# Kernel tuning notes

Hardware: AMD Instinct MI355X
Metric: run time of the kernel (lower is better)

The kernel has to match this reference:

```python
import jax, jax.numpy as jnp
import numpy as np

N_TRAIN = 2000
N_ATOMS = 21
DIM_D = N_ATOMS * (N_ATOMS - 1) // 2   # 210 pairwise descriptors
DIM_I = 3 * N_ATOMS                    # 63 Cartesian force dims
N_PERMS = 12
N_COLS = 8
SIG = 10.0

_TRIL_ROWS, _TRIL_COLS = np.tril_indices(N_ATOMS, k=-1)


def setup_inputs() -> dict:
    key = jax.random.key(0)
    k1, k2 = jax.random.split(key)
    R_desc = jax.random.normal(k1, (N_TRAIN, DIM_D), dtype=jnp.float32)
    R_d_desc = jax.random.normal(k2, (N_TRAIN, DIM_D, 3), dtype=jnp.float32)
    rng = np.random.default_rng(0)
    # permutation table: identity first, then random symmetry perms of descriptor rows
    perms = np.stack([np.arange(DIM_D)] + [rng.permutation(DIM_D) for _ in range(N_PERMS - 1)])  # (P, D)
    # linear indices into a tiled (P copies) descriptor, laid out so that
    # tril_perms_lin.reshape(DIM_D, N_PERMS)[k, p] = perms[p, k] + p*DIM_D (matches sGDML)
    tril_perms_lin = (perms.T + np.arange(N_PERMS)[None, :] * DIM_D).ravel()
    j_idxs = rng.integers(0, N_TRAIN, size=N_COLS)
    return {
        "R_desc": R_desc,
        "R_d_desc": R_d_desc,
        "tril_perms_lin": jnp.asarray(tril_perms_lin, dtype=jnp.int32),
        "j_idxs": jnp.asarray(j_idxs, dtype=jnp.int32),
    }


def _d_desc_full(d_comp):
    """Expand compact pairwise Jacobian (N, D, 3) to full (N, D, 3*A).
    Pair row k for atoms (a,b) gets +d in atom a's slot and -d in atom b's slot."""
    n = d_comp.shape[0]
    out = jnp.zeros((n, DIM_D, N_ATOMS, 3), d_comp.dtype)
    k = jnp.arange(DIM_D)
    out = out.at[:, k, _TRIL_ROWS].set(d_comp)
    out = out.at[:, k, _TRIL_COLS].set(-d_comp)
    return out.reshape(n, DIM_D, DIM_I)


def reference(R_desc, R_d_desc, tril_perms_lin, j_idxs):
    sqrt5 = np.sqrt(5.0).astype(np.float32)
    base_div = 3.0 * SIG ** 4
    # indexing a P-fold tiled array of length D is equivalent to mod D
    perm_idx = jnp.reshape(tril_perms_lin, (DIM_D, N_PERMS)).T % DIM_D  # (P, D)
    Rd_full = _d_desc_full(R_d_desc)  # (N, D, I)

    def column_block(j):
        rj_desc_perms = R_desc[j][perm_idx]        # (P, D)  permuted descriptor of point j
        rj_d_perms = Rd_full[j][perm_idx]          # (P, D, I) permuted Jacobian of point j
        diff = R_desc[:, None, :] - rj_desc_perms[None, :, :]   # (N, P, D)
        norm = sqrt5 * jnp.linalg.norm(diff, axis=-1)            # (N, P)
        mat52 = jnp.exp(-norm / SIG) * (5.0 / base_div)          # (N, P)
        b = jnp.einsum('npd,pde->npe', diff, rj_d_perms)         # (N, P, I)
        outer = jnp.einsum('npd,npe->nde', diff * (5.0 * mat52)[..., None], b)  # (N, D, I)
        outer = outer - jnp.einsum('pde,np->nde', rj_d_perms, (SIG ** 2 + SIG * norm) * mat52)
        kblk = jnp.einsum('nde,ndk->nke', outer, Rd_full)        # (N, I_row, I_col)
        return kblk.reshape(N_TRAIN * DIM_I, DIM_I)

    K = jax.vmap(column_block)(j_idxs)                 # (nJ, N*I, I)
    K = jnp.transpose(K, (1, 0, 2)).reshape(N_TRAIN * DIM_I, N_COLS * DIM_I)
    return K
```

## Files before the change

### kernel.cpp

```cpp
#include <hip/hip_runtime.h>
#include <hip/hip_fp16.h>
#include <math.h>

#define NTRAIN 2000
#define DIMD 210
#define DIMI 63
#define NPERM 12
#define NCOLS 8
#define NATOM 21
#define SIGF 10.0f

#define WS_PERM      0
#define WS_PAIRROW   5040
#define WS_PAIRCOL   5250
#define WS_GTAB      6300
#define WS_ENTOFF    11340
#define WS_ENTS      11782
#define WS_TILEMAP   21862
#define WS_PERMAB    22304
#define A_INT_OFF    25088
#define A_BYTE_OFF   (A_INT_OFF * 4)
#define A_PER_N      (64 * 224)
#define A_BYTES      ((size_t)NTRAIN * A_PER_N * 2)
#define WS_NEEDED    ((size_t)A_BYTE_OFF + A_BYTES)

typedef _Float16 f16x8 __attribute__((ext_vector_type(8)));
typedef float f32x4 __attribute__((ext_vector_type(4)));

__global__ __launch_bounds__(512) void gdml_setup(const int* __restrict__ tril,
                                                  int* __restrict__ ws, int wsBig) {
  __shared__ int sPerm[NPERM * DIMD];
  __shared__ int sInv[NPERM * DIMD];
  __shared__ int sRow[DIMD], sCol[DIMD];
  __shared__ int sPairs[NATOM * 20], sNeg[NATOM * 20];
  __shared__ int sCnt[441];
  __shared__ int sScan[512];
  __shared__ int sOff[442];

  const int tid = threadIdx.x;

  for (int d = tid; d < DIMD; d += 512) {
    int a = 1;
    while ((a * (a + 1)) / 2 <= d) a++;
    sRow[d] = a;
    sCol[d] = d - (a * (a - 1)) / 2;
  }
  for (int idx = tid; idx < NPERM * DIMD; idx += 512) {
    int p = idx / DIMD, d = idx % DIMD;
    sPerm[idx] = tril[d * NPERM + p] % DIMD;
  }
  __syncthreads();
  for (int idx = tid; idx < NPERM * DIMD; idx += 512) {
    int p = idx / DIMD;
    sInv[p * DIMD + sPerm[idx]] = idx % DIMD;
  }
  if (tid < NATOM) {
    int t = tid, c = 0;
    for (int d = 0; d < DIMD; ++d) {
      if (sRow[d] == t)      { sPairs[t * 20 + c] = d; sNeg[t * 20 + c] = 0; c++; }
      else if (sCol[d] == t) { sPairs[t * 20 + c] = d; sNeg[t * 20 + c] = 1; c++; }
    }
  }
  __syncthreads();

  for (int idx = tid; idx < NPERM * NATOM * 20; idx += 512) {
    int p = idx / (NATOM * 20);
    int r = idx % (NATOM * 20);
    int d = sPairs[r], neg = sNeg[r];
    int tw = sInv[p * DIMD + d];
    int pd = sPerm[p * DIMD + d];
    ws[WS_GTAB + idx] = d | (tw << 9) | (pd << 18) | (neg << 27);
  }

  if (wsBig) {
    for (int idx = tid; idx < NPERM * DIMD; idx += 512) {
      int dd = sPerm[idx];
      ws[WS_PERMAB + idx] = dd | (sRow[dd] << 8) | (sCol[dd] << 13);
    }
    return;
  }

  for (int idx = tid; idx < NPERM * DIMD; idx += 512) ws[WS_PERM + idx] = sPerm[idx];

  for (int q = tid; q < 441; q += 512) {
    int A = q / NATOM, B = q % NATOM, c = 0;
    for (int i = 0; i < 20; ++i) {
      int d = sPairs[A * 20 + i];
      for (int p = 0; p < NPERM; ++p) {
        int dd = sPerm[p * DIMD + d];
        c += (sRow[dd] == B) + (sCol[dd] == B);
      }
    }
    sCnt[q] = c;
  }
  __syncthreads();

  sScan[tid] = (tid < 441) ? sCnt[tid] : 0;
  __syncthreads();
  for (int s = 1; s < 512; s <<= 1) {
    int v = (tid >= s) ? sScan[tid - s] : 0;
    __syncthreads();
    sScan[tid] += v;
    __syncthreads();
  }
  if (tid == 0) sOff[0] = 0;
  if (tid < 441) sOff[tid + 1] = sScan[tid];
  __syncthreads();
  for (int q = tid; q < 442; q += 512) ws[WS_ENTOFF + q] = sOff[q];

  for (int q = tid; q < 441; q += 512) {
    int c = sCnt[q], r = 0;
    for (int q2 = 0; q2 < 441; ++q2) {
      int c2v = sCnt[q2];
      r += (c2v > c) || (c2v == c && q2 < q);
    }
    ws[WS_TILEMAP + r] = q;
  }

  for (int q = tid; q < 441; q += 512) {
    int A = q / NATOM, B = q % NATOM;
    int o = sOff[q];
    for (int i = 0; i < 20; ++i) {
      int d = sPairs[A * 20 + i];
      int negA = sNeg[A * 20 + i];
      for (int p = 0; p < NPERM; ++p) {
        int dd = sPerm[p * DIMD + d];
        int base = (d << 3) | (dd << 15) | (p << 26);
        if (sRow[dd] == B) ws[WS_ENTS + (o++)] = base | ((negA ^ 1) << 30);
        if (sCol[dd] == B) ws[WS_ENTS + (o++)] = base | (negA << 30);
      }
    }
  }
}

__global__ __launch_bounds__(256) void build_A(const float* __restrict__ R_d_desc,
                                               int* __restrict__ ws) {
  const int bid = blockIdx.x;
  const int n = (bid & 7) * (NTRAIN / 8) + (bid >> 3);
  const int* gtab = ws + WS_GTAB;
  _Float16* A = (_Float16*)((char*)ws + A_BYTE_OFF) + (size_t)n * A_PER_N;
  const float* rd = R_d_desc + (size_t)n * (DIMD * 3);
  const int tid = threadIdx.x;

  f16x8 z = {0, 0, 0, 0, 0, 0, 0, 0};
  for (int u = tid; u < 64 * 28; u += 256) ((f16x8*)A)[u] = z;
  __syncthreads();

  for (int u = tid; u < NATOM * 20; u += 256) {
    int v = gtab[u];
    int d = v & 511;
    float s = (v & (1 << 27)) ? -1.0f : 1.0f;
    int at = u / 20;
    A[(3 * at + 0) * 224 + d] = (_Float16)(s * rd[3 * d + 0]);
    A[(3 * at + 1) * 224 + d] = (_Float16)(s * rd[3 * d + 1]);
    A[(3 * at + 2) * 224 + d] = (_Float16)(s * rd[3 * d + 2]);
  }
}

__device__ inline unsigned h16(float f) {
  return (unsigned)__half_as_ushort(__float2half_rn(f));
}
__device__ inline float uh(unsigned u) {
  return __half2float(__ushort_as_half((unsigned short)(u & 0xFFFFu)));
}
__device__ inline int tswz(int r, int e) {
  return r * 64 + ((((e >> 3) ^ r) & 7) << 3) + (e & 7);
}
__device__ inline float pick3(uint2 v, int u) {
  return (u == 0) ? uh(v.x) : (u == 1) ? uh(v.x >> 16) : uh(v.y);
}

#define MT_STRIDE 232

__global__ __launch_bounds__(256, 4) void gdml_main_mfma(
    const float* __restrict__ R_desc, const float* __restrict__ R_d_desc,
    const int* __restrict__ j_idxs, const int* __restrict__ ws,
    float* __restrict__ out) {
  const int* gtab   = ws + WS_GTAB;
  const int* permAB = ws + WS_PERMAB;

  const int bid = blockIdx.x;
  const int x = bid & 7;
  const int t = bid >> 3;
  const int n = x * (NTRAIN / 8) + (t >> 3);
  const int jc = t & 7;
  const int tid = threadIdx.x;
  const int j = j_idxs[jc];

  __shared__ __align__(16) _Float16 MT[64 * MT_STRIDE];
  __shared__ uint2 Rdn2[DIMD];
  __shared__ uint2 Rdj2[DIMD];
  __shared__ __align__(16) _Float16 Gk[64][16];
  __shared__ float c1s[NPERM], c2s[NPERM];
  __shared__ float2 RnRj[DIMD];
  __shared__ float partial[252];

  if (tid < DIMD) {
    RnRj[tid] = make_float2(R_desc[(size_t)n * DIMD + tid],
                            R_desc[(size_t)j * DIMD + tid]);
    const float* gn = R_d_desc + (size_t)n * (DIMD * 3) + 3 * tid;
    const float* gj = R_d_desc + (size_t)j * (DIMD * 3) + 3 * tid;
    Rdn2[tid] = make_uint2(h16(gn[0]) | (h16(gn[1]) << 16), h16(gn[2]));
    Rdj2[tid] = make_uint2(h16(gj[0]) | (h16(gj[1]) << 16), h16(gj[2]));
  }
  {
    float4 zf = make_float4(0.f, 0.f, 0.f, 0.f);
    float4* mz = (float4*)MT;
    for (int i = tid; i < 64 * MT_STRIDE * 2 / 16; i += 256) mz[i] = zf;
    f16x8 z8 = {0, 0, 0, 0, 0, 0, 0, 0};
    for (int i = tid; i < 128; i += 256) ((f16x8*)Gk)[i] = z8;
  }
  __syncthreads();

  float g0 = 0, g1 = 0, g2 = 0, b0 = 0, b1 = 0, b2 = 0;
  int bp = 0, bat = 0;
  if (tid < NPERM * NATOM) {
    bp = tid / NATOM; bat = tid - bp * NATOM;
    const int* gt = &gtab[(bp * NATOM + bat) * 20];
    float nacc = 0.f;
#pragma unroll
    for (int i = 0; i < 20; ++i) {
      int v = gt[i];
      int d = v & 511, tw = (v >> 9) & 511, pd = (v >> 18) & 511;
      unsigned sg = ((unsigned)(v & (1 << 27))) << 4;
      float2 rrd = RnRj[d];
      float diff_d = rrd.x - RnRj[pd].y;
      float diff_tw = RnRj[tw].x - rrd.y;
      float fd = __uint_as_float(__float_as_uint(diff_d) ^ sg);
      float ftw = __uint_as_float(__float_as_uint(diff_tw) ^ sg);
      nacc += diff_d * diff_d;
      uint2 rn = Rdn2[d];
      uint2 rj = Rdj2[d];
      g0 += uh(rn.x) * fd;  g1 += uh(rn.x >> 16) * fd;  g2 += uh(rn.y) * fd;
      b0 += uh(rj.x) * ftw; b1 += uh(rj.x >> 16) * ftw; b2 += uh(rj.y) * ftw;
    }
    partial[tid] = nacc;
  }
  __syncthreads();

  if (tid < NPERM) {
    float s = 0.f;
#pragma unroll
    for (int i = 0; i < 21; ++i) s += partial[tid * 21 + i];
    s *= 0.5f;
    float nrm = sqrtf(5.0f) * sqrtf(s);
    float mat52 = expf(-nrm / SIGF) * (5.0f / (3.0f * SIGF * SIGF * SIGF * SIGF));
    c1s[tid] = 5.0f * mat52;
    c2s[tid] = (SIGF * SIGF + SIGF * nrm) * mat52;
  }
  __syncthreads();

  if (tid < NPERM * NATOM) {
    float c1 = c1s[bp];
    Gk[3 * bat + 0][4 + bp] = (_Float16)(c1 * g0);
    Gk[3 * bat + 1][4 + bp] = (_Float16)(c1 * g1);
    Gk[3 * bat + 2][4 + bp] = (_Float16)(c1 * g2);
    MT[(3 * bat + 0) * MT_STRIDE + 212 + bp] = (_Float16)b0;
    MT[(3 * bat + 1) * MT_STRIDE + 212 + bp] = (_Float16)b1;
    MT[(3 * bat + 2) * MT_STRIDE + 212 + bp] = (_Float16)b2;
  }
  if (tid < DIMD) {
    int d = tid;
    _Float16* m = MT + d;
#pragma unroll
    for (int p = 0; p < NPERM; ++p) {
      int v = permAB[p * DIMD + d];
      int dd = v & 255, a = (v >> 8) & 31, b = (v >> 13) & 31;
      float c2 = c2s[p];
      uint2 rj = Rdj2[dd];
      float v0 = c2 * uh(rj.x), v1 = c2 * uh(rj.x >> 16), v2 = c2 * uh(rj.y);
      int ca = (3 * a) * MT_STRIDE, cb = (3 * b) * MT_STRIDE;
      m[ca] = (_Float16)((float)m[ca] - v0);
      m[ca + MT_STRIDE] = (_Float16)((float)m[ca + MT_STRIDE] - v1);
      m[ca + 2 * MT_STRIDE] = (_Float16)((float)m[ca + 2 * MT_STRIDE] - v2);
      m[cb] = (_Float16)((float)m[cb] + v0);
      m[cb + MT_STRIDE] = (_Float16)((float)m[cb + MT_STRIDE] + v1);
      m[cb + 2 * MT_STRIDE] = (_Float16)((float)m[cb + 2 * MT_STRIDE] + v2);
    }
  } else {
    for (int r = tid - DIMD; r < DIMI; r += 256 - DIMD) {
      int at = r / 3, u = r - 3 * at;
      float v208 = (at == 20) ? pick3(Rdn2[208], u)
                 : (at == 18) ? -pick3(Rdn2[208], u) : 0.f;
      float v209 = (at == 20) ? pick3(Rdn2[209], u)
                 : (at == 19) ? -pick3(Rdn2[209], u) : 0.f;
      Gk[r][0] = (_Float16)v208;
      Gk[r][1] = (_Float16)v209;
    }
  }
  __syncthreads();

  f32x4 acc0 = {0.f, 0.f, 0.f, 0.f}, acc1 = acc0, acc2 = acc0, acc3 = acc0;
  const int lane = tid & 63;
  const int nt = tid >> 6;
  const int ci = lane & 15;
  const int kOct = lane >> 4;
  const _Float16* Ag = (const _Float16*)((const char*)ws + A_BYTE_OFF)
                       + (size_t)n * A_PER_N;
  const _Float16* aBase = Ag + ci * 224 + kOct * 8;
  const _Float16* mBase = &MT[(16 * nt + ci) * MT_STRIDE + kOct * 8];
  {
    f16x8 bf_c = *(const f16x8*)(mBase);
    f16x8 a0_c = *(const f16x8*)(aBase);
    f16x8 a1_c = *(const f16x8*)(aBase + 16 * 224);
    f16x8 a2_c = *(const f16x8*)(aBase + 32 * 224);
    f16x8 a3_c = *(const f16x8*)(aBase + 48 * 224);
#pragma unroll
    for (int kk = 0; kk < 6; ++kk) {
      f16x8 bf_n, a0_n, a1_n, a2_n, a3_n;
      if (kk < 5) {
        bf_n = *(const f16x8*)(mBase + (kk + 1) * 32);
        a0_n = *(const f16x8*)(aBase + (kk + 1) * 32);
        a1_n = *(const f16x8*)(aBase + 16 * 224 + (kk + 1) * 32);
        a2_n = *(const f16x8*)(aBase + 32 * 224 + (kk + 1) * 32);
        a3_n = *(const f16x8*)(aBase + 48 * 224 + (kk + 1) * 32);
      }
      acc0 = __builtin_amdgcn_mfma_f32_16x16x32_f16(a0_c, bf_c, acc0, 0, 0, 0);
      acc1 = __builtin_amdgcn_mfma_f32_16x16x32_f16(a1_c, bf_c, acc1, 0, 0, 0);
      acc2 = __builtin_amdgcn_mfma_f32_16x16x32_f16(a2_c, bf_c, acc2, 0, 0, 0);
      acc3 = __builtin_amdgcn_mfma_f32_16x16x32_f16(a3_c, bf_c, acc3, 0, 0, 0);
      if (kk < 5) {
        bf_c = bf_n; a0_c = a0_n; a1_c = a1_n; a2_c = a2_n; a3_c = a3_n;
      }
    }
    f16x8 bf6 = *(const f16x8*)(mBase + 6 * 32);
    f16x8 a0, a1, a2, a3;
    if (kOct >= 2) {
      int off = (kOct - 2) * 8;
      a0 = *(const f16x8*)&Gk[ci][off];
      a1 = *(const f16x8*)&Gk[16 + ci][off];
      a2 = *(const f16x8*)&Gk[32 + ci][off];
      a3 = *(const f16x8*)&Gk[48 + ci][off];
    } else {
      a0 = *(const f16x8*)(aBase + 6 * 32);
      a1 = *(const f16x8*)(aBase + 16 * 224 + 6 * 32);
      a2 = *(const f16x8*)(aBase + 32 * 224 + 6 * 32);
      a3 = *(const f16x8*)(aBase + 48 * 224 + 6 * 32);
    }
    acc0 = __builtin_amdgcn_mfma_f32_16x16x32_f16(a0, bf6, acc0, 0, 0, 0);
    acc1 = __builtin_amdgcn_mfma_f32_16x16x32_f16(a1, bf6, acc1, 0, 0, 0);
    acc2 = __builtin_amdgcn_mfma_f32_16x16x32_f16(a2, bf6, acc2, 0, 0, 0);
    acc3 = __builtin_amdgcn_mfma_f32_16x16x32_f16(a3, bf6, acc3, 0, 0, 0);
  }

  {
    const int c = 16 * nt + ci;
    if (c < DIMI) {
      const size_t base = (size_t)n * DIMI * (NCOLS * DIMI) + (size_t)jc * DIMI;
      float* ob = out + base + c;
      const int rb = kOct * 4;
#pragma unroll
      for (int r8 = 0; r8 < 4; ++r8) {
        int r = rb + r8;
        ob[(size_t)r * (NCOLS * DIMI)] = acc0[r8];
        ob[(size_t)(16 + r) * (NCOLS * DIMI)] = acc1[r8];
        ob[(size_t)(32 + r) * (NCOLS * DIMI)] = acc2[r8];
        if (48 + r < DIMI) ob[(size_t)(48 + r) * (NCOLS * DIMI)] = acc3[r8];
      }
    }
  }
}

__global__ __launch_bounds__(256, 8) void gdml_main_csr(
    const float* __restrict__ R_desc, const float* __restrict__ R_d_desc,
    const int* __restrict__ j_idxs, const int* __restrict__ ws,
    float* __restrict__ out) {
  const int* perm    = ws + WS_PERM;
  const int* gtab    = ws + WS_GTAB;
  const int* entOff  = ws + WS_ENTOFF;
  const int* ents    = ws + WS_ENTS;
  const int* tileMap = ws + WS_TILEMAP;

  const int bid = blockIdx.x;
  const int jc = bid & 7;
  const int n = bid >> 3;
  const int tid = threadIdx.x;
  const int j = j_idxs[jc];

  __shared__ uint2 Rdn2[DIMD];
  __shared__ uint2 Rdj2[DIMD];
  __shared__ __align__(16) float GT[NPERM][64];
  __shared__ __align__(16) float bT[NPERM][64];
  __shared__ float c1s[NPERM], c2s[NPERM];
  __shared__ __align__(16) char uni[DIMI * 64 * 2];
  float* Rn = (float*)uni;
  float* Rj = Rn + DIMD;
  float* partial = Rj + DIMD;
  ushort* tileH = (ushort*)uni;

  for (int i = tid; i < DIMD; i += 256) {
    Rn[i] = R_desc[(size_t)n * DIMD + i];
    Rj[i] = R_desc[(size_t)j * DIMD + i];
  }
  if (tid < DIMD) {
    const float* gn = R_d_desc + (size_t)n * (DIMD * 3) + 3 * tid;
    const float* gj = R_d_desc + (size_t)j * (DIMD * 3) + 3 * tid;
    Rdn2[tid] = make_uint2(h16(gn[0]) | (h16(gn[1]) << 16), h16(gn[2]));
    Rdj2[tid] = make_uint2(h16(gj[0]) | (h16(gj[1]) << 16), h16(gj[2]));
  }
  __syncthreads();

  if (tid < 252) {
    int p = tid / 21, seg = tid % 21;
    const int* pp = &perm[p * DIMD + seg * 10];
    const float* rn = &Rn[seg * 10];
    float s = 0.f;
#pragma unroll
    for (int i = 0; i < 10; ++i) {
      float v = rn[i] - Rj[pp[i]];
      s += v * v;
    }
    partial[tid] = s;
  }
  __syncthreads();
  if (tid < NPERM) {
    float s = 0.f;
#pragma unroll
    for (int i = 0; i < 21; ++i) s += partial[tid * 21 + i];
    float nrm = sqrtf(5.0f) * sqrtf(s);
    float mat52 = expf(-nrm / SIGF) * (5.0f / (3.0f * SIGF * SIGF * SIGF * SIGF));
    c1s[tid] = 5.0f * mat52;
    c2s[tid] = (SIGF * SIGF + SIGF * nrm) * mat52;
  }
  __syncthreads();

  if (tid < NPERM * NATOM) {
    int p = tid / NATOM, at = tid % NATOM;
    const int* gt = &gtab[(p * NATOM + at) * 20];
    float g0 = 0, g1 = 0, g2 = 0, b0 = 0, b1 = 0, b2 = 0;
#pragma unroll
    for (int i = 0; i < 20; ++i) {
      int v = gt[i];
      int d = v & 511, tw = (v >> 9) & 511, pd = (v >> 18) & 511;
      unsigned sg = ((unsigned)(v & (1 << 27))) << 4;
      float fd = __uint_as_float(__float_as_uint(Rn[d] - Rj[pd]) ^ sg);
      float ftw = __uint_as_float(__float_as_uint(Rn[tw] - Rj[d]) ^ sg);
      uint2 rn = Rdn2[d];
      uint2 rj = Rdj2[d];
      g0 += uh(rn.x) * fd;  g1 += uh(rn.x >> 16) * fd;  g2 += uh(rn.y) * fd;
      b0 += uh(rj.x) * ftw; b1 += uh(rj.x >> 16) * ftw; b2 += uh(rj.y) * ftw;
    }
    float c1 = c1s[p];
    GT[p][3 * at + 0] = c1 * g0;
    GT[p][3 * at + 1] = c1 * g1;
    GT[p][3 * at + 2] = c1 * g2;
    bT[p][3 * at + 0] = b0;
    bT[p][3 * at + 1] = b1;
    bT[p][3 * at + 2] = b2;
  }
  __syncthreads();

  for (int s = 0; s < 2; ++s) {
    int rank;
    if (s == 0) { if (tid > 220) break; rank = tid; }
    else        { if (tid >= 220) break; rank = 440 - tid; }
    int q = tileMap[rank];
    int A = q / NATOM, B = q % NATOM;
    float acc[3][3];
#pragma unroll
    for (int c = 0; c < 3; ++c)
#pragma unroll
      for (int e = 0; e < 3; ++e) acc[c][e] = 0.f;

    int o0 = entOff[q], o1 = entOff[q + 1];
    for (int o = o0; o < o1; ++o) {
      int v = ents[o];
      int d8  = v & 0xFF8;
      int dd8 = (v >> 12) & 0xFF8;
      int p4  = (v >> 24) & 0x3C;
      unsigned sgn = ((unsigned)v & 0x40000000u) << 1;
      float c2 = __uint_as_float(
          __float_as_uint(*(const float*)((const char*)c2s + p4)) ^ sgn);
      uint2 rn = *(const uint2*)((const char*)Rdn2 + d8);
      uint2 rj = *(const uint2*)((const char*)Rdj2 + dd8);
      float nx = uh(rn.x), ny = uh(rn.x >> 16), nz = uh(rn.y);
      float w0 = c2 * uh(rj.x), w1 = c2 * uh(rj.x >> 16), w2 = c2 * uh(rj.y);
      acc[0][0] += nx * w0; acc[0][1] += nx * w1; acc[0][2] += nx * w2;
      acc[1][0] += ny * w0; acc[1][1] += ny * w1; acc[1][2] += ny * w2;
      acc[2][0] += nz * w0; acc[2][1] += nz * w1; acc[2][2] += nz * w2;
    }
#pragma unroll
    for (int cg = 0; cg < 3; ++cg) {
      int r = 3 * A + cg;
#pragma unroll
      for (int u = 0; u < 3; ++u)
        tileH[tswz(r, 3 * B + u)] = (ushort)h16(acc[cg][u]);
    }
  }
  __syncthreads();

  const size_t base = (size_t)n * DIMI * (NCOLS * DIMI) + (size_t)jc * DIMI;
  if (tid < 252) {
    int k = tid >> 2, ec = tid & 3;
    int e0 = ec * 16;
    const uint4* q0 = (const uint4*)&tileH[k * 64 + (((2 * ec) ^ k) & 7) * 8];
    const uint4* q1 = (const uint4*)&tileH[k * 64 + (((2 * ec + 1) ^ k) & 7) * 8];
    uint4 u0 = *q0, u1 = *q1;
    float acc[16];
    acc[0] = uh(u0.x);  acc[1] = uh(u0.x >> 16);
    acc[2] = uh(u0.y);  acc[3] = uh(u0.y >> 16);
    acc[4] = uh(u0.z);  acc[5] = uh(u0.z >> 16);
    acc[6] = uh(u0.w);  acc[7] = uh(u0.w >> 16);
    acc[8] = uh(u1.x);  acc[9] = uh(u1.x >> 16);
    acc[10] = uh(u1.y); acc[11] = uh(u1.y >> 16);
    acc[12] = uh(u1.z); acc[13] = uh(u1.z >> 16);
    acc[14] = uh(u1.w); acc[15] = uh(u1.w >> 16);
#pragma unroll
    for (int p = 0; p < NPERM; ++p) {
      float g = GT[p][k];
      const float4* bp = (const float4*)&bT[p][e0];
      float4 b0 = bp[0], b1 = bp[1], b2 = bp[2], b3 = bp[3];
      acc[0] += g * b0.x;  acc[1] += g * b0.y;  acc[2] += g * b0.z;  acc[3] += g * b0.w;
      acc[4] += g * b1.x;  acc[5] += g * b1.y;  acc[6] += g * b1.z;  acc[7] += g * b1.w;
      acc[8] += g * b2.x;  acc[9] += g * b2.y;  acc[10] += g * b2.z; acc[11] += g * b2.w;
      acc[12] += g * b3.x; acc[13] += g * b3.y; acc[14] += g * b3.z; acc[15] += g * b3.w;
    }
    float* op = out + base + (size_t)k * (NCOLS * DIMI) + e0;
    const int lim = DIMI - e0;
#pragma unroll
    for (int i = 0; i < 16; ++i)
      if (i < lim) op[i] = acc[i];
  }
}

extern "C" void kernel_launch(void* const* d_in, const int* in_sizes, int n_in,
                              void* d_out, int out_size, void* d_ws, size_t ws_size,
                              hipStream_t stream) {
  const float* R_desc = (const float*)d_in[0];
  const float* R_d_desc = (const float*)d_in[1];
  const int* tril = (const int*)d_in[2];
  const int* j_idxs = (const int*)d_in[3];
  float* out = (float*)d_out;
  int* ws = (int*)d_ws;

  const int wsBig = (ws_size >= WS_NEEDED) ? 1 : 0;
  hipLaunchKernelGGL(gdml_setup, dim3(1), dim3(512), 0, stream, tril, ws, wsBig);
  if (wsBig) {
    hipLaunchKernelGGL(build_A, dim3(NTRAIN), dim3(256), 0, stream, R_d_desc, ws);
    hipLaunchKernelGGL(gdml_main_mfma, dim3(NTRAIN * NCOLS), dim3(256), 0, stream,
                       R_desc, R_d_desc, j_idxs, ws, out);
  } else {
    hipLaunchKernelGGL(gdml_main_csr, dim3(NTRAIN * NCOLS), dim3(256), 0, stream,
                       R_desc, R_d_desc, j_idxs, ws, out);
  }
}
```

Measured before the change: 282.1 us.

## Compute permuted G and B projections with MFMA instead of scalar gather loops

The per-permutation projections g (diff times the Jacobian of n) and b (permuted diff times the Jacobian of j) are now built as small matrix products on the MFMA units. The kernel first stores fp16 diff and permuted-diff tiles in shared memory, then multiplies them against the precomputed expanded Jacobian tables. Before, each thread ran a 20-step gather over a pair table in scalar code. The change reuses the MT buffer for the diff tiles, so it adds extra zeroing passes and barriers. It also drops the Rdn2 staging and the manual software prefetch in the main MFMA loop, and it adds fp16 rounding of the diffs before the projections.

```diff
diff --git a/kernel.cpp b/kernel.cpp
--- a/kernel.cpp
+++ b/kernel.cpp
@@ -11,8 +11,6 @@
 #define SIGF 10.0f
 
 #define WS_PERM      0
-#define WS_PAIRROW   5040
-#define WS_PAIRCOL   5250
 #define WS_GTAB      6300
 #define WS_ENTOFF    11340
 #define WS_ENTS      11782
@@ -74,6 +72,7 @@
 
   if (wsBig) {
     for (int idx = tid; idx < NPERM * DIMD; idx += 512) {
+      ws[WS_PERM + idx] = sPerm[idx] | (sInv[idx] << 9);
       int dd = sPerm[idx];
       ws[WS_PERMAB + idx] = dd | (sRow[dd] << 8) | (sCol[dd] << 13);
     }
@@ -166,17 +165,15 @@
 __device__ inline int tswz(int r, int e) {
   return r * 64 + ((((e >> 3) ^ r) & 7) << 3) + (e & 7);
 }
-__device__ inline float pick3(uint2 v, int u) {
-  return (u == 0) ? uh(v.x) : (u == 1) ? uh(v.x >> 16) : uh(v.y);
-}
 
 #define MT_STRIDE 232
+#define DIF_HALVES (16 * MT_STRIDE)
 
 __global__ __launch_bounds__(256, 4) void gdml_main_mfma(
     const float* __restrict__ R_desc, const float* __restrict__ R_d_desc,
     const int* __restrict__ j_idxs, const int* __restrict__ ws,
     float* __restrict__ out) {
-  const int* gtab   = ws + WS_GTAB;
+  const int* ptab   = ws + WS_PERM;
   const int* permAB = ws + WS_PERMAB;
 
   const int bid = blockIdx.x;
@@ -188,51 +185,48 @@
   const int j = j_idxs[jc];
 
   __shared__ __align__(16) _Float16 MT[64 * MT_STRIDE];
-  __shared__ uint2 Rdn2[DIMD];
+  _Float16* Dif  = MT;
+  _Float16* DifP = MT + DIF_HALVES;
   __shared__ uint2 Rdj2[DIMD];
   __shared__ __align__(16) _Float16 Gk[64][16];
   __shared__ float c1s[NPERM], c2s[NPERM];
   __shared__ float2 RnRj[DIMD];
   __shared__ float partial[252];
 
+  const _Float16* Atab = (const _Float16*)((const char*)ws + A_BYTE_OFF);
+
   if (tid < DIMD) {
     RnRj[tid] = make_float2(R_desc[(size_t)n * DIMD + tid],
                             R_desc[(size_t)j * DIMD + tid]);
-    const float* gn = R_d_desc + (size_t)n * (DIMD * 3) + 3 * tid;
     const float* gj = R_d_desc + (size_t)j * (DIMD * 3) + 3 * tid;
-    Rdn2[tid] = make_uint2(h16(gn[0]) | (h16(gn[1]) << 16), h16(gn[2]));
     Rdj2[tid] = make_uint2(h16(gj[0]) | (h16(gj[1]) << 16), h16(gj[2]));
   }
   {
-    float4 zf = make_float4(0.f, 0.f, 0.f, 0.f);
-    float4* mz = (float4*)MT;
-    for (int i = tid; i < 64 * MT_STRIDE * 2 / 16; i += 256) mz[i] = zf;
     f16x8 z8 = {0, 0, 0, 0, 0, 0, 0, 0};
     for (int i = tid; i < 128; i += 256) ((f16x8*)Gk)[i] = z8;
-  }
-  __syncthreads();
-
-  float g0 = 0, g1 = 0, g2 = 0, b0 = 0, b1 = 0, b2 = 0;
-  int bp = 0, bat = 0;
-  if (tid < NPERM * NATOM) {
-    bp = tid / NATOM; bat = tid - bp * NATOM;
-    const int* gt = &gtab[(bp * NATOM + bat) * 20];
+    for (int i = tid; i < 352; i += 256) {
+      int a = i / 176, rem = i - a * 176;
+      int p = rem / 11, tt = rem - p * 11;
+      int off = a * DIF_HALVES + p * MT_STRIDE + 210 + 2 * tt;
+      *(unsigned*)((char*)MT + 2 * off) = 0u;
+    }
+  }
+  __syncthreads();
+
+  if (tid < 252) {
+    int p = tid / 21, seg = tid - 21 * (tid / 21);
     float nacc = 0.f;
 #pragma unroll
-    for (int i = 0; i < 20; ++i) {
-      int v = gt[i];
-      int d = v & 511, tw = (v >> 9) & 511, pd = (v >> 18) & 511;
-      unsigned sg = ((unsigned)(v & (1 << 27))) << 4;
-      float2 rrd = RnRj[d];
-      float diff_d = rrd.x - RnRj[pd].y;
-      float diff_tw = RnRj[tw].x - rrd.y;
-      float fd = __uint_as_float(__float_as_uint(diff_d) ^ sg);
-      float ftw = __uint_as_float(__float_as_uint(diff_tw) ^ sg);
-      nacc += diff_d * diff_d;
-      uint2 rn = Rdn2[d];
-      uint2 rj = Rdj2[d];
-      g0 += uh(rn.x) * fd;  g1 += uh(rn.x >> 16) * fd;  g2 += uh(rn.y) * fd;
-      b0 += uh(rj.x) * ftw; b1 += uh(rj.x >> 16) * ftw; b2 += uh(rj.y) * ftw;
+    for (int i = 0; i < 10; ++i) {
+      int d = seg * 10 + i;
+      int v = ptab[p * DIMD + d];
+      int pd = v & 511, tw = (v >> 9) & 511;
+      float2 rr = RnRj[d];
+      float di = rr.x - RnRj[pd].y;
+      float dp = RnRj[tw].x - rr.y;
+      Dif[p * MT_STRIDE + d] = (_Float16)di;
+      DifP[p * MT_STRIDE + d] = (_Float16)dp;
+      nacc += di * di;
     }
     partial[tid] = nacc;
   }
@@ -242,22 +236,61 @@
     float s = 0.f;
 #pragma unroll
     for (int i = 0; i < 21; ++i) s += partial[tid * 21 + i];
-    s *= 0.5f;
     float nrm = sqrtf(5.0f) * sqrtf(s);
     float mat52 = expf(-nrm / SIGF) * (5.0f / (3.0f * SIGF * SIGF * SIGF * SIGF));
     c1s[tid] = 5.0f * mat52;
     c2s[tid] = (SIGF * SIGF + SIGF * nrm) * mat52;
   }
-  __syncthreads();
-
-  if (tid < NPERM * NATOM) {
-    float c1 = c1s[bp];
-    Gk[3 * bat + 0][4 + bp] = (_Float16)(c1 * g0);
-    Gk[3 * bat + 1][4 + bp] = (_Float16)(c1 * g1);
-    Gk[3 * bat + 2][4 + bp] = (_Float16)(c1 * g2);
-    MT[(3 * bat + 0) * MT_STRIDE + 212 + bp] = (_Float16)b0;
-    MT[(3 * bat + 1) * MT_STRIDE + 212 + bp] = (_Float16)b1;
-    MT[(3 * bat + 2) * MT_STRIDE + 212 + bp] = (_Float16)b2;
+  {
+    float4 zf = make_float4(0.f, 0.f, 0.f, 0.f);
+    float4* mz = (float4*)(MT + 2 * DIF_HALVES);
+    for (int i = tid; i < 928; i += 256) mz[i] = zf;
+  }
+  __syncthreads();
+
+  const int lane = tid & 63;
+  const int w = tid >> 6;
+  const int ci = lane & 15;
+  const int kOct = lane >> 4;
+  f32x4 accG = {0.f, 0.f, 0.f, 0.f}, accB = accG;
+  {
+    const _Float16* An = Atab + (size_t)n * A_PER_N + (16 * w + ci) * 224 + kOct * 8;
+    const _Float16* Aj = Atab + (size_t)j * A_PER_N + (16 * w + ci) * 224 + kOct * 8;
+    const _Float16* Db = Dif + ci * MT_STRIDE + kOct * 8;
+    const _Float16* Pb = DifP + ci * MT_STRIDE + kOct * 8;
+#pragma unroll
+    for (int kk = 0; kk < 7; ++kk) {
+      f16x8 bg = *(const f16x8*)(Db + kk * 32);
+      f16x8 bb = *(const f16x8*)(Pb + kk * 32);
+      f16x8 an = *(const f16x8*)(An + kk * 32);
+      f16x8 aj = *(const f16x8*)(Aj + kk * 32);
+      accG = __builtin_amdgcn_mfma_f32_16x16x32_f16(an, bg, accG, 0, 0, 0);
+      accB = __builtin_amdgcn_mfma_f32_16x16x32_f16(aj, bb, accB, 0, 0, 0);
+    }
+  }
+  if (ci < NPERM) {
+    float c1 = c1s[ci];
+#pragma unroll
+    for (int r8 = 0; r8 < 4; ++r8) {
+      int krow = 16 * w + kOct * 4 + r8;
+      Gk[krow][4 + ci] = (_Float16)(c1 * accG[r8]);
+    }
+  }
+  __syncthreads();
+
+  {
+    float4 zf = make_float4(0.f, 0.f, 0.f, 0.f);
+    float4* mz = (float4*)MT;
+    for (int i = tid; i < 928; i += 256) mz[i] = zf;
+  }
+  __syncthreads();
+
+  if (ci < NPERM) {
+#pragma unroll
+    for (int r8 = 0; r8 < 4; ++r8) {
+      int e = 16 * w + kOct * 4 + r8;
+      MT[e * MT_STRIDE + 212 + ci] = (_Float16)accB[r8];
+    }
   }
   if (tid < DIMD) {
     int d = tid;
@@ -278,12 +311,12 @@
       m[cb + 2 * MT_STRIDE] = (_Float16)((float)m[cb + 2 * MT_STRIDE] + v2);
     }
   } else {
+    const float* rdn = R_d_desc + (size_t)n * (DIMD * 3);
     for (int r = tid - DIMD; r < DIMI; r += 256 - DIMD) {
       int at = r / 3, u = r - 3 * at;
-      float v208 = (at == 20) ? pick3(Rdn2[208], u)
-                 : (at == 18) ? -pick3(Rdn2[208], u) : 0.f;
-      float v209 = (at == 20) ? pick3(Rdn2[209], u)
-                 : (at == 19) ? -pick3(Rdn2[209], u) : 0.f;
+      float r208 = rdn[3 * 208 + u], r209 = rdn[3 * 209 + u];
+      float v208 = (at == 20) ? r208 : (at == 18) ? -r208 : 0.f;
+      float v209 = (at == 20) ? r209 : (at == 19) ? -r209 : 0.f;
       Gk[r][0] = (_Float16)v208;
       Gk[r][1] = (_Float16)v209;
     }
@@ -291,37 +324,22 @@
   __syncthreads();
 
   f32x4 acc0 = {0.f, 0.f, 0.f, 0.f}, acc1 = acc0, acc2 = acc0, acc3 = acc0;
-  const int lane = tid & 63;
-  const int nt = tid >> 6;
-  const int ci = lane & 15;
-  const int kOct = lane >> 4;
-  const _Float16* Ag = (const _Float16*)((const char*)ws + A_BYTE_OFF)
-                       + (size_t)n * A_PER_N;
-  const _Float16* aBase = Ag + ci * 224 + kOct * 8;
-  const _Float16* mBase = &MT[(16 * nt + ci) * MT_STRIDE + kOct * 8];
+  const int nt = w;
   {
-    f16x8 bf_c = *(const f16x8*)(mBase);
-    f16x8 a0_c = *(const f16x8*)(aBase);
-    f16x8 a1_c = *(const f16x8*)(aBase + 16 * 224);
-    f16x8 a2_c = *(const f16x8*)(aBase + 32 * 224);
-    f16x8 a3_c = *(const f16x8*)(aBase + 48 * 224);
+    const _Float16* Ag = Atab + (size_t)n * A_PER_N;
+    const _Float16* aBase = Ag + ci * 224 + kOct * 8;
+    const _Float16* mBase = &MT[(16 * nt + ci) * MT_STRIDE + kOct * 8];
 #pragma unroll
     for (int kk = 0; kk < 6; ++kk) {
-      f16x8 bf_n, a0_n, a1_n, a2_n, a3_n;
-      if (kk < 5) {
-        bf_n = *(const f16x8*)(mBase + (kk + 1) * 32);
-        a0_n = *(const f16x8*)(aBase + (kk + 1) * 32);
-        a1_n = *(const f16x8*)(aBase + 16 * 224 + (kk + 1) * 32);
-        a2_n = *(const f16x8*)(aBase + 32 * 224 + (kk + 1) * 32);
-        a3_n = *(const f16x8*)(aBase + 48 * 224 + (kk + 1) * 32);
-      }
-      acc0 = __builtin_amdgcn_mfma_f32_16x16x32_f16(a0_c, bf_c, acc0, 0, 0, 0);
-      acc1 = __builtin_amdgcn_mfma_f32_16x16x32_f16(a1_c, bf_c, acc1, 0, 0, 0);
-      acc2 = __builtin_amdgcn_mfma_f32_16x16x32_f16(a2_c, bf_c, acc2, 0, 0, 0);
-      acc3 = __builtin_amdgcn_mfma_f32_16x16x32_f16(a3_c, bf_c, acc3, 0, 0, 0);
-      if (kk < 5) {
-        bf_c = bf_n; a0_c = a0_n; a1_c = a1_n; a2_c = a2_n; a3_c = a3_n;
-      }
+      f16x8 bf = *(const f16x8*)(mBase + kk * 32);
+      f16x8 a0 = *(const f16x8*)(aBase + kk * 32);
+      f16x8 a1 = *(const f16x8*)(aBase + 16 * 224 + kk * 32);
+      f16x8 a2 = *(const f16x8*)(aBase + 32 * 224 + kk * 32);
+      f16x8 a3 = *(const f16x8*)(aBase + 48 * 224 + kk * 32);
+      acc0 = __builtin_amdgcn_mfma_f32_16x16x32_f16(a0, bf, acc0, 0, 0, 0);
+      acc1 = __builtin_amdgcn_mfma_f32_16x16x32_f16(a1, bf, acc1, 0, 0, 0);
+      acc2 = __builtin_amdgcn_mfma_f32_16x16x32_f16(a2, bf, acc2, 0, 0, 0);
+      acc3 = __builtin_amdgcn_mfma_f32_16x16x32_f16(a3, bf, acc3, 0, 0, 0);
     }
     f16x8 bf6 = *(const f16x8*)(mBase + 6 * 32);
     f16x8 a0, a1, a2, a3;
```

New measurement: 321.7 us. 14.0% more time.
